# Performance work log

Measured on AMD Instinct MI355X. Metric: run time of the kernel, lower is better.

Reference implementation:

```python
import jax, jax.numpy as jnp
import numpy as np

B, D = 8192, 1024

def setup_inputs() -> dict:
    key = jax.random.key(0)
    ks = jax.random.split(key, 5)
    scale = 1.0 / np.sqrt(D)
    return {
        "x": jax.random.normal(ks[0], (B, D), dtype=jnp.float32),
        "h": jax.random.normal(ks[1], (B, D), dtype=jnp.float32),
        "c": jax.random.normal(ks[2], (B, D), dtype=jnp.float32),
        # gate order: [input, forget, output, candidate]
        "Wx": jax.random.normal(ks[3], (4, D, D), dtype=jnp.float32) * scale,
        "Wh": jax.random.normal(ks[4], (4, D, D), dtype=jnp.float32) * scale,
    }

def reference(x, h, c, Wx, Wh):
    # two batched GEMMs covering all 8 projections: [B,D] x [4,D,D] -> [4,B,D]
    gx = jnp.einsum('bd,gdk->gbk', x, Wx)
    gh = jnp.einsum('bd,gdk->gbk', h, Wh)
    g = gx + gh
    i = jax.nn.sigmoid(g[0])
    f = jax.nn.sigmoid(g[1])
    o = jax.nn.sigmoid(g[2])
    u = jnp.tanh(g[3])
    c_t = i * u + f * c
    h_t = o * jnp.tanh(c_t)
    return (h_t, c_t)
```

## Files before the change

kernel.cpp:

```cpp
#include <hip/hip_runtime.h>
#include <hip/hip_bf16.h>
#include <cstdint>


#define LDS_TOTAL 131072

typedef __attribute__((ext_vector_type(8))) short bf16x8;
typedef __attribute__((ext_vector_type(16))) float f32x16;
typedef __attribute__((ext_vector_type(4))) unsigned int u32x4;

static __device__ __forceinline__ unsigned short f2bf(float f) {
  union { float f; unsigned int u; } v; v.f = f;
  unsigned int u = v.u;
  unsigned int r = (u + 0x7FFFu + ((u >> 16) & 1u)) >> 16;
  return (unsigned short)r;
}

static __device__ __forceinline__ void load16(const void* gp, void* lp) {
  __builtin_amdgcn_global_load_lds(
      (const __attribute__((address_space(1))) void*)gp,
      (__attribute__((address_space(3))) void*)lp, 16, 0, 0);
}

static __device__ __forceinline__ float sigmoid_f(float x) {
  return 1.0f / (1.0f + __expf(-x));
}
static __device__ __forceinline__ float tanh_f(float x) {
  float e = __expf(-2.0f * fabsf(x));
  float r = (1.0f - e) / (1.0f + e);
  return copysignf(r, x);
}

__global__ __launch_bounds__(256) void prep_fused_kernel(
    const float* __restrict__ x, const float* __restrict__ h,
    const float* __restrict__ Wx, const float* __restrict__ Wh,
    unsigned short* __restrict__ Ap, unsigned short* __restrict__ Wt2) {
  __shared__ float tile[64][65];
  const int r = threadIdx.x >> 4;
  const int c4 = (threadIdx.x & 15) << 2;
  if (blockIdx.x < 4096) {
    const int b0 = (blockIdx.x >> 5) << 6;
    const int k0 = (blockIdx.x & 31) << 6;
    const float* src; int ks;
    if (k0 < 1024) { src = x; ks = k0; } else { src = h; ks = k0 - 1024; }
    #pragma unroll
    for (int s = 0; s < 4; ++s) {
      float4 v = *(const float4*)(src + (size_t)(b0 + s * 16 + r) * 1024 + ks + c4);
      tile[s * 16 + r][c4 + 0] = v.x; tile[s * 16 + r][c4 + 1] = v.y;
      tile[s * 16 + r][c4 + 2] = v.z; tile[s * 16 + r][c4 + 3] = v.w;
    }
    __syncthreads();
    #pragma unroll
    for (int i = 0; i < 2; ++i) {
      int cc = i * 256 + threadIdx.x;
      int kb = cc >> 6, bb = cc & 63;
      union { unsigned short s[8]; u32x4 v; } o;
      #pragma unroll
      for (int e = 0; e < 8; ++e) o.s[e] = f2bf(tile[bb][kb * 8 + e]);
      *(u32x4*)(Ap + ((size_t)((k0 >> 3) + kb) * 8192 + b0 + bb) * 8) = o.v;
    }
  } else {
    const int bid = blockIdx.x - 4096;
    const int g = bid >> 9;
    const int kt = (bid >> 4) & 31;
    const int nt = bid & 15;
    const int k0 = kt << 6, n0 = nt << 6;
    const float* W; int ks;
    if (k0 < 1024) { W = Wx + (size_t)g * 1048576; ks = k0; }
    else           { W = Wh + (size_t)g * 1048576; ks = k0 - 1024; }
    #pragma unroll
    for (int s = 0; s < 4; ++s) {
      float4 v = *(const float4*)(W + (size_t)(ks + s * 16 + r) * 1024 + n0 + c4);
      tile[s * 16 + r][c4 + 0] = v.x; tile[s * 16 + r][c4 + 1] = v.y;
      tile[s * 16 + r][c4 + 2] = v.z; tile[s * 16 + r][c4 + 3] = v.w;
    }
    __syncthreads();
    #pragma unroll
    for (int i = 0; i < 2; ++i) {
      int cc = i * 256 + threadIdx.x;
      int kb = cc >> 6, nn = cc & 63;
      union { unsigned short s[8]; u32x4 v; } o;
      #pragma unroll
      for (int e = 0; e < 8; ++e) o.s[e] = f2bf(tile[kb * 8 + e][nn]);
      *(u32x4*)(Wt2 + ((size_t)((k0 >> 3) + kb) * 4096 + g * 1024 + n0 + nn) * 8) = o.v;
    }
  }
}

#define VMW(n) asm volatile("s_waitcnt vmcnt(" #n ")" ::: "memory")
#define LGKM0() asm volatile("s_waitcnt lgkmcnt(0)" ::: "memory")
#define BAR() __builtin_amdgcn_s_barrier()

__global__ __launch_bounds__(512, 2) void lstm_gemm_kernel(
    const unsigned short* __restrict__ Ap,
    const unsigned short* __restrict__ Wt2,
    const float* __restrict__ cprev,
    float* __restrict__ out) {
  extern __shared__ char lds[];
  const int tid = threadIdx.x;
  const int l = tid & 63;
  const int w = tid >> 6;
  const int wr = w >> 1;
  const int wc = w & 1;
  const int bid = blockIdx.x;
  const int xcd = bid & 7;
  const int cc = bid >> 3;
  const int nt = xcd * 2 + (cc >> 5);
  const int mt = cc & 31;
  const int m0 = mt << 8;
  const int n0 = nt << 6;

  char* const buf0 = lds;
  char* const buf1 = lds + 65536;

  f32x16 acc[2][4];
  #pragma unroll
  for (int mf = 0; mf < 2; ++mf)
    #pragma unroll
    for (int g = 0; g < 4; ++g) acc[mf][g] = (f32x16)0.0f;

  const int ln = l & 31;
  const int hl = l >> 5;

  const int aBase = hl * 4096 + (wr * 64 + ln) * 16;
  const int bBase = 32768 + hl * 1024 + (wc * 32 + ln) * 16;

  const unsigned short* const gA =
      Ap + (size_t)(tid >> 8) * 65536 + (size_t)(m0 + (tid & 255)) * 8;
  const unsigned short* const gB =
      Wt2 + (size_t)((tid >> 6) & 1) * 32768 +
      (size_t)((tid >> 7) * 1024 + n0 + (tid & 63)) * 8;
  const int dA = (tid & ~63) << 4;
  const int dB = 32768 + ((tid & ~63) << 4);

  auto stPair = [&](char* buf, int j, int t) {
    load16(gA + (size_t)(t * 8 + j * 2) * 65536, buf + j * 8192 + dA);
    load16(gB + (size_t)(t * 8 + j * 2) * 32768, buf + j * 8192 + dB);
  };

  bf16x8 a_[2][2], b_[2][4];
  auto rd2 = [&](const char* bufc, int h) {
    #pragma unroll
    for (int r = 0; r < 2; ++r) {
      const char* pb = bufc + (2 * h + r) * 8192;
      a_[r][0] = *(const bf16x8*)(pb + aBase);
      a_[r][1] = *(const bf16x8*)(pb + aBase + 512);
      b_[r][0] = *(const bf16x8*)(pb + bBase);
      b_[r][1] = *(const bf16x8*)(pb + bBase + 2048);
      b_[r][2] = *(const bf16x8*)(pb + bBase + 4096);
      b_[r][3] = *(const bf16x8*)(pb + bBase + 6144);
    }
  };
  auto mfma2 = [&]() {
    __builtin_amdgcn_s_setprio(1);
    #pragma unroll
    for (int r = 0; r < 2; ++r)
      #pragma unroll
      for (int mf = 0; mf < 2; ++mf)
        #pragma unroll
        for (int g = 0; g < 4; ++g)
          acc[mf][g] = __builtin_amdgcn_mfma_f32_32x32x16_bf16(
              a_[r][mf], b_[r][g], acc[mf][g], 0, 0, 0);
    __builtin_amdgcn_s_setprio(0);
  };

  #pragma unroll
  for (int j = 0; j < 4; ++j) stPair(buf0, j, 0);
  stPair(buf1, 0, 1); stPair(buf1, 1, 1);
  VMW(4);
  BAR();

  #pragma unroll 1
  for (int t = 0; t < 30; ++t) {
    char* bufc = lds + ((t & 1) << 16);
    char* bufn = lds + (((t + 1) & 1) << 16);
    rd2(bufc, 0);
    stPair(bufn, 2, t + 1); stPair(bufn, 3, t + 1);
    VMW(8); BAR(); LGKM0();
    mfma2();
    BAR();
    rd2(bufc, 1);
    stPair(bufc, 0, t + 2); stPair(bufc, 1, t + 2);
    VMW(8); BAR(); LGKM0();
    mfma2();
    BAR();
  }
  rd2(buf0, 0); stPair(buf1, 2, 31); stPair(buf1, 3, 31);
  VMW(8); BAR(); LGKM0(); mfma2(); BAR();
  rd2(buf0, 1);
  VMW(4); BAR(); LGKM0(); mfma2(); BAR();
  rd2(buf1, 0);
  VMW(0); BAR(); LGKM0(); mfma2(); BAR();
  rd2(buf1, 1);
  LGKM0(); mfma2();

  const int colB = n0 + wc * 32 + ln;
  #pragma unroll
  for (int mf = 0; mf < 2; ++mf) {
    #pragma unroll
    for (int r = 0; r < 16; ++r) {
      int row = m0 + wr * 64 + mf * 32 + (r & 3) + ((r >> 2) << 3) + (hl << 2);
      float gi = acc[mf][0][r];
      float gf = acc[mf][1][r];
      float go = acc[mf][2][r];
      float gu = acc[mf][3][r];
      float i_ = sigmoid_f(gi);
      float f_ = sigmoid_f(gf);
      float o_ = sigmoid_f(go);
      float u_ = tanh_f(gu);
      size_t idx = (size_t)row * 1024 + colB;
      float ct = i_ * u_ + f_ * cprev[idx];
      float ht = o_ * tanh_f(ct);
      out[idx] = ht;
      out[8388608 + idx] = ct;
    }
  }
}

extern "C" void kernel_launch(void* const* d_in, const int* in_sizes, int n_in,
                              void* d_out, int out_size, void* d_ws, size_t ws_size,
                              hipStream_t stream) {
  const float* x  = (const float*)d_in[0];
  const float* h  = (const float*)d_in[1];
  const float* c  = (const float*)d_in[2];
  const float* Wx = (const float*)d_in[3];
  const float* Wh = (const float*)d_in[4];
  float* out = (float*)d_out;

  unsigned short* Ap  = (unsigned short*)d_ws;
  unsigned short* Wt2 = (unsigned short*)((char*)d_ws + 33554432);

  hipFuncSetAttribute((const void*)lstm_gemm_kernel,
                      hipFuncAttributeMaxDynamicSharedMemorySize, LDS_TOTAL);

  prep_fused_kernel<<<6144, 256, 0, stream>>>(x, h, Wx, Wh, Ap, Wt2);
  lstm_gemm_kernel<<<dim3(512), dim3(512), LDS_TOTAL, stream>>>(Ap, Wt2, c, out);
}
```

Measured before the change: 167.0 us.

## Retile LSTM GEMM to 128x32 blocks with 16x16 MFMA and triple buffering

Restructures the fused LSTM GEMM from 512-thread blocks computing 256x64 tiles with 32x32x16 MFMA and a double-buffered 64KB pipeline into 256-thread blocks computing 128x32 tiles with 16x16x32 MFMA and a three-stage 16KB ring buffer. Smaller LDS use (48KB) and launch bounds of 3 blocks per CU aim to raise occupancy and overlap loads with compute using a single barrier per K step. In exchange, the smaller tiles lower arithmetic intensity and increase global traffic for reloading A and W across more blocks.

```diff
diff --git a/kernel.cpp b/kernel.cpp
--- a/kernel.cpp
+++ b/kernel.cpp
@@ -3,10 +3,10 @@
 #include <cstdint>
 
 
-#define LDS_TOTAL 131072
+#define LDS_TOTAL 49152
 
 typedef __attribute__((ext_vector_type(8))) short bf16x8;
-typedef __attribute__((ext_vector_type(16))) float f32x16;
+typedef __attribute__((ext_vector_type(4))) float f32x4;
 typedef __attribute__((ext_vector_type(4))) unsigned int u32x4;
 
 static __device__ __forceinline__ unsigned short f2bf(float f) {
@@ -91,7 +91,7 @@
 #define LGKM0() asm volatile("s_waitcnt lgkmcnt(0)" ::: "memory")
 #define BAR() __builtin_amdgcn_s_barrier()
 
-__global__ __launch_bounds__(512, 2) void lstm_gemm_kernel(
+__global__ __launch_bounds__(256, 3) void lstm_gemm_kernel(
     const unsigned short* __restrict__ Ap,
     const unsigned short* __restrict__ Wt2,
     const float* __restrict__ cprev,
@@ -105,110 +105,91 @@
   const int bid = blockIdx.x;
   const int xcd = bid & 7;
   const int cc = bid >> 3;
-  const int nt = xcd * 2 + (cc >> 5);
-  const int mt = cc & 31;
-  const int m0 = mt << 8;
-  const int n0 = nt << 6;
-
-  char* const buf0 = lds;
-  char* const buf1 = lds + 65536;
-
-  f32x16 acc[2][4];
+  const int nt = xcd * 4 + (cc >> 6);
+  const int mt = cc & 63;
+  const int m0 = mt << 7;
+  const int n0 = nt << 5;
+
+  f32x4 acc[4][4];
   #pragma unroll
-  for (int mf = 0; mf < 2; ++mf)
-    #pragma unroll
-    for (int g = 0; g < 4; ++g) acc[mf][g] = (f32x16)0.0f;
-
-  const int ln = l & 31;
-  const int hl = l >> 5;
-
-  const int aBase = hl * 4096 + (wr * 64 + ln) * 16;
-  const int bBase = 32768 + hl * 1024 + (wc * 32 + ln) * 16;
+  for (int mf = 0; mf < 4; ++mf)
+    #pragma unroll
+    for (int g = 0; g < 4; ++g) acc[mf][g] = (f32x4)0.0f;
+
+  const int lr = l & 15;
+  const int kb4 = l >> 4;
+
+  const int aBase = kb4 * 2048 + (wr * 64 + lr) * 16;
+  const int bBase = 8192 + kb4 * 2048 + (wc * 16 + lr) * 16;
 
   const unsigned short* const gA =
-      Ap + (size_t)(tid >> 8) * 65536 + (size_t)(m0 + (tid & 255)) * 8;
+      Ap + (size_t)(tid >> 7) * 65536 + (size_t)(m0 + (tid & 127)) * 8;
   const unsigned short* const gB =
-      Wt2 + (size_t)((tid >> 6) & 1) * 32768 +
-      (size_t)((tid >> 7) * 1024 + n0 + (tid & 63)) * 8;
+      Wt2 + (size_t)(tid >> 7) * 32768 + (size_t)((tid >> 5) & 3) * 8192 +
+      (size_t)(n0 + (tid & 31)) * 8;
   const int dA = (tid & ~63) << 4;
-  const int dB = 32768 + ((tid & ~63) << 4);
-
-  auto stPair = [&](char* buf, int j, int t) {
-    load16(gA + (size_t)(t * 8 + j * 2) * 65536, buf + j * 8192 + dA);
-    load16(gB + (size_t)(t * 8 + j * 2) * 32768, buf + j * 8192 + dB);
+  const int dB = 8192 + dA;
+
+  auto stage = [&](int bo, int t) {
+    const unsigned short* a0 = gA + (size_t)t * 262144;
+    load16(a0,          lds + bo + dA);
+    load16(a0 + 131072, lds + bo + dA + 4096);
+    const unsigned short* b0 = gB + (size_t)t * 131072;
+    load16(b0,          lds + bo + dB);
+    load16(b0 + 65536,  lds + bo + dB + 4096);
   };
 
-  bf16x8 a_[2][2], b_[2][4];
-  auto rd2 = [&](const char* bufc, int h) {
-    #pragma unroll
-    for (int r = 0; r < 2; ++r) {
-      const char* pb = bufc + (2 * h + r) * 8192;
-      a_[r][0] = *(const bf16x8*)(pb + aBase);
-      a_[r][1] = *(const bf16x8*)(pb + aBase + 512);
-      b_[r][0] = *(const bf16x8*)(pb + bBase);
-      b_[r][1] = *(const bf16x8*)(pb + bBase + 2048);
-      b_[r][2] = *(const bf16x8*)(pb + bBase + 4096);
-      b_[r][3] = *(const bf16x8*)(pb + bBase + 6144);
-    }
+  bf16x8 aR[4], bR[4];
+  auto rd8 = [&](int bo) {
+    const char* p = lds + bo;
+    aR[0] = *(const bf16x8*)(p + aBase);
+    aR[1] = *(const bf16x8*)(p + aBase + 256);
+    aR[2] = *(const bf16x8*)(p + aBase + 512);
+    aR[3] = *(const bf16x8*)(p + aBase + 768);
+    bR[0] = *(const bf16x8*)(p + bBase);
+    bR[1] = *(const bf16x8*)(p + bBase + 512);
+    bR[2] = *(const bf16x8*)(p + bBase + 1024);
+    bR[3] = *(const bf16x8*)(p + bBase + 1536);
   };
-  auto mfma2 = [&]() {
+
+  int bo0 = 0, bo1 = 16384, bo2 = 32768;
+  stage(bo0, 0);
+  stage(bo1, 1);
+
+  #pragma unroll 1
+  for (int t = 0; t < 64; ++t) {
+    if (t < 62) { VMW(4); } else { VMW(0); }
+    BAR();
+    if (t + 2 < 64) stage(bo2, t + 2);
+    rd8(bo0);
+    LGKM0();
     __builtin_amdgcn_s_setprio(1);
     #pragma unroll
-    for (int r = 0; r < 2; ++r)
+    for (int mf = 0; mf < 4; ++mf)
       #pragma unroll
-      for (int mf = 0; mf < 2; ++mf)
-        #pragma unroll
-        for (int g = 0; g < 4; ++g)
-          acc[mf][g] = __builtin_amdgcn_mfma_f32_32x32x16_bf16(
-              a_[r][mf], b_[r][g], acc[mf][g], 0, 0, 0);
+      for (int g = 0; g < 4; ++g)
+        acc[mf][g] = __builtin_amdgcn_mfma_f32_16x16x32_bf16(
+            aR[mf], bR[g], acc[mf][g], 0, 0, 0);
     __builtin_amdgcn_s_setprio(0);
-  };
-
+    int tmp = bo0; bo0 = bo1; bo1 = bo2; bo2 = tmp;
+  }
+
+  const int q = (l >> 4) << 2;
+  const int col = n0 + wc * 16 + lr;
   #pragma unroll
-  for (int j = 0; j < 4; ++j) stPair(buf0, j, 0);
-  stPair(buf1, 0, 1); stPair(buf1, 1, 1);
-  VMW(4);
-  BAR();
-
-  #pragma unroll 1
-  for (int t = 0; t < 30; ++t) {
-    char* bufc = lds + ((t & 1) << 16);
-    char* bufn = lds + (((t + 1) & 1) << 16);
-    rd2(bufc, 0);
-    stPair(bufn, 2, t + 1); stPair(bufn, 3, t + 1);
-    VMW(8); BAR(); LGKM0();
-    mfma2();
-    BAR();
-    rd2(bufc, 1);
-    stPair(bufc, 0, t + 2); stPair(bufc, 1, t + 2);
-    VMW(8); BAR(); LGKM0();
-    mfma2();
-    BAR();
-  }
-  rd2(buf0, 0); stPair(buf1, 2, 31); stPair(buf1, 3, 31);
-  VMW(8); BAR(); LGKM0(); mfma2(); BAR();
-  rd2(buf0, 1);
-  VMW(4); BAR(); LGKM0(); mfma2(); BAR();
-  rd2(buf1, 0);
-  VMW(0); BAR(); LGKM0(); mfma2(); BAR();
-  rd2(buf1, 1);
-  LGKM0(); mfma2();
-
-  const int colB = n0 + wc * 32 + ln;
-  #pragma unroll
-  for (int mf = 0; mf < 2; ++mf) {
-    #pragma unroll
-    for (int r = 0; r < 16; ++r) {
-      int row = m0 + wr * 64 + mf * 32 + (r & 3) + ((r >> 2) << 3) + (hl << 2);
-      float gi = acc[mf][0][r];
-      float gf = acc[mf][1][r];
-      float go = acc[mf][2][r];
-      float gu = acc[mf][3][r];
+  for (int mf = 0; mf < 4; ++mf) {
+    #pragma unroll
+    for (int j = 0; j < 4; ++j) {
+      int row = m0 + wr * 64 + mf * 16 + q + j;
+      float gi = acc[mf][0][j];
+      float gf = acc[mf][1][j];
+      float go = acc[mf][2][j];
+      float gu = acc[mf][3][j];
       float i_ = sigmoid_f(gi);
       float f_ = sigmoid_f(gf);
       float o_ = sigmoid_f(go);
       float u_ = tanh_f(gu);
-      size_t idx = (size_t)row * 1024 + colB;
+      size_t idx = (size_t)row * 1024 + col;
       float ct = i_ * u_ + f_ * cprev[idx];
       float ht = o_ * tanh_f(ct);
       out[idx] = ht;
@@ -230,9 +211,6 @@
   unsigned short* Ap  = (unsigned short*)d_ws;
   unsigned short* Wt2 = (unsigned short*)((char*)d_ws + 33554432);
 
-  hipFuncSetAttribute((const void*)lstm_gemm_kernel,
-                      hipFuncAttributeMaxDynamicSharedMemorySize, LDS_TOTAL);
-
   prep_fused_kernel<<<6144, 256, 0, stream>>>(x, h, Wx, Wh, Ap, Wt2);
-  lstm_gemm_kernel<<<dim3(512), dim3(512), LDS_TOTAL, stream>>>(Ap, Wt2, c, out);
-}
+  lstm_gemm_kernel<<<dim3(2048), dim3(256), LDS_TOTAL, stream>>>(Ap, Wt2, c, out);
+}
```

After: 189.1 us. 13.3% more time.
